# Performance work log

Measured on AMD Instinct MI355X. Metric: run time of the kernel, lower is better.

The kernel has to match this reference:

```python
import jax, jax.numpy as jnp
import numpy as np

B, D, K, A = 32768, 256, 1024, 32
MIN_LOG_STD, MAX_LOG_STD = -20.0, 2.0


def setup_inputs() -> dict:
    key = jax.random.key(0)
    ks = jax.random.split(key, 9)
    return {
        "obs": jax.random.normal(ks[0], (B, D), dtype=jnp.float32),
        "mean_C": jax.random.normal(ks[1], (K, D), dtype=jnp.float32),
        "mean_sigma": jnp.abs(jax.random.normal(ks[2], (K,), dtype=jnp.float32)) + 0.1,
        "mean_w": jax.random.normal(ks[3], (A, K), dtype=jnp.float32),
        "mean_b": jax.random.normal(ks[4], (A,), dtype=jnp.float32),
        "std_C": jax.random.normal(ks[5], (K, D), dtype=jnp.float32),
        "std_sigma": jnp.abs(jax.random.normal(ks[6], (K,), dtype=jnp.float32)) + 0.1,
        "std_w": jax.random.normal(ks[7], (A, K), dtype=jnp.float32),
        "std_b": jax.random.normal(ks[8], (A,), dtype=jnp.float32),
    }


def _rbf(x, C, sigma_sq, w, b):
    # r[b,k] = sum_d (x[b,d] - C[k,d])^2, expanded to avoid a [B,K,D] intermediate
    x2 = jnp.sum(x * x, axis=-1, keepdims=True)           # [B,1]
    c2 = jnp.sum(C * C, axis=-1)[None, :]                  # [1,K]
    r = x2 - 2.0 * (x @ C.T) + c2                          # [B,K]
    phi = jnp.exp(-r / (2.0 * jnp.abs(sigma_sq)[None, :]))  # [B,K]
    return phi @ w.T + b[None, :]                          # [B,A]


def reference(obs, mean_C, mean_sigma, mean_w, mean_b,
              std_C, std_sigma, std_w, std_b):
    action_mean = _rbf(obs, mean_C, mean_sigma, mean_w, mean_b)
    std_raw = _rbf(obs, std_C, std_sigma, std_w, std_b)
    action_std = jnp.exp(jnp.clip(std_raw, MIN_LOG_STD, MAX_LOG_STD))
    return jnp.concatenate((action_mean, action_std), axis=-1)  # [B, 2A]
```

## Files before the change

kernel.cpp:

```cpp
#include <hip/hip_runtime.h>


typedef float floatx4 __attribute__((ext_vector_type(4)));
typedef unsigned int u32;
typedef unsigned char u8;

constexpr float LOG2E = 1.4426950408889634f;

__device__ __forceinline__ u32 pk_fp8(float a, float b, float c, float d) {
  u32 v = __builtin_amdgcn_cvt_pk_fp8_f32(a, b, 0u, 0);
  v = __builtin_amdgcn_cvt_pk_fp8_f32(c, d, v, 1);
  return v;
}
__device__ __forceinline__ long mk64(u32 lo, u32 hi) {
  return (long)lo | ((long)hi << 32);
}

__global__ void prep(const float* __restrict__ mC, const float* __restrict__ mS,
                     const float* __restrict__ sC, const float* __restrict__ sS,
                     const float* __restrict__ mw, const float* __restrict__ sw,
                     u8* __restrict__ Cb, float* __restrict__ a2g,
                     float* __restrict__ g2n, u8* __restrict__ wb)
{
  const int blk = blockIdx.x;
  if (blk < 512) {
    const int wv = threadIdx.x >> 6;
    const int l  = threadIdx.x & 63;
    const int b  = blk * 4 + wv;
    const int half = b >> 10;
    const int k = b & 1023;
    const float* src = (half ? sC : mC) + (size_t)k * 256;
    float4 f = *(const float4*)(src + l * 4);
    float ss = f.x*f.x + f.y*f.y + f.z*f.z + f.w*f.w;
    ((u32*)Cb)[b * 64 + l] = pk_fp8(f.x, f.y, f.z, f.w);
    for (int off = 32; off > 0; off >>= 1) ss += __shfl_down(ss, off, 64);
    if (l == 0) {
      float sig = fabsf((half ? sS : mS)[k]);
      float s2 = LOG2E * 0.5f / sig;
      a2g[b] = 2.f * s2;
      g2n[b] = -s2 * ss;
    }
  } else {
    int i0 = (blk - 512) * 1024 + threadIdx.x * 4;
    int half = i0 >> 15;
    int rem  = i0 & 32767;
    const float* src = half ? sw : mw;
    float4 f = *(const float4*)(src + rem);
    ((u32*)wb)[i0 >> 2] = pk_fp8(f.x, f.y, f.z, f.w);
  }
}

__global__ __launch_bounds__(256, 2)
void policy_main(const float* __restrict__ obs,
                 const u8* __restrict__ Cb,
                 const float* __restrict__ a2g,
                 const float* __restrict__ g2n,
                 const u8* __restrict__ wb,
                 const float* __restrict__ mbias,
                 const float* __restrict__ sbias,
                 float* __restrict__ out)
{
  __shared__ __align__(16) char smem[69888];
  float* x2p = (float*)(smem + 65536);
  float* red = (float*)smem;

  const int tid  = threadIdx.x;
  const int lane = tid & 63;
  const int wv   = tid >> 6;
  const int c    = lane & 15;
  const int q    = lane >> 4;
  const int row0 = blockIdx.x * 64;
  const int crow = 16 * wv + c;
  const int kslc = 16 * wv + 4 * q;
  const int ldl  = tid * 16;

  int goff[4];
  #pragma unroll
  for (int i = 0; i < 4; ++i) {
    int s = i * 256 + tid;
    int row = s >> 4;
    int l16 = (s & 15) ^ (row & 15);
    goff[i] = row * 256 + l16 * 16;
  }

  #pragma unroll
  for (int i = 0; i < 4; ++i) {
    __builtin_amdgcn_global_load_lds(
        (const __attribute__((address_space(1))) u32*)(const void*)(Cb + goff[i]),
        (__attribute__((address_space(3))) u32*)(void*)(smem + i * 4096 + ldl), 16, 0, 0);
    __builtin_amdgcn_global_load_lds(
        (const __attribute__((address_space(1))) u32*)(const void*)(Cb + 16384 + goff[i]),
        (__attribute__((address_space(3))) u32*)(void*)(smem + 16384 + i * 4096 + ldl), 16, 0, 0);
  }

  #pragma unroll
  for (int i = 0; i < 4; ++i) {
    int s = i * 256 + tid;
    int row = s >> 4;
    int s16 = s & 15;
    int l16 = s16 ^ (row & 15);
    const float* src = obs + (size_t)(row0 + row) * 256 + l16 * 16;
    float4 f0 = ((const float4*)src)[0];
    float4 f1 = ((const float4*)src)[1];
    float4 f2 = ((const float4*)src)[2];
    float4 f3 = ((const float4*)src)[3];
    uint4 pk;
    pk.x = pk_fp8(f0.x, f0.y, f0.z, f0.w);
    pk.y = pk_fp8(f1.x, f1.y, f1.z, f1.w);
    pk.z = pk_fp8(f2.x, f2.y, f2.z, f2.w);
    pk.w = pk_fp8(f3.x, f3.y, f3.z, f3.w);
    *(uint4*)(smem + 49152 + s * 16) = pk;
    float p = f0.x*f0.x + f0.y*f0.y + f0.z*f0.z + f0.w*f0.w
            + f1.x*f1.x + f1.y*f1.y + f1.z*f1.z + f1.w*f1.w
            + f2.x*f2.x + f2.y*f2.y + f2.z*f2.z + f2.w*f2.w
            + f3.x*f3.x + f3.y*f3.y + f3.z*f3.z + f3.w*f3.w;
    x2p[row * 16 + s16] = p;
  }
  __syncthreads();

  long ob[4][8];
  #pragma unroll
  for (int nt = 0; nt < 4; ++nt) {
    const int row = nt * 16 + c;
    #pragma unroll
    for (int ks = 0; ks < 8; ++ks) {
      int cc8 = 4 * ks + q;
      int s16 = (cc8 >> 1) ^ (row & 15);
      ob[nt][ks] = *(const long*)(smem + 49152 + row * 256 + s16 * 16 + (q & 1) * 8);
    }
  }
  if (tid < 64) {
    float s = 0.f;
    #pragma unroll
    for (int j = 0; j < 16; j += 4) {
      float4 a = *(const float4*)(x2p + tid * 16 + j);
      s += a.x + a.y + a.z + a.w;
    }
    x2p[1024 + tid] = s;
  }
  __syncthreads();

  float hx2[4];
  #pragma unroll
  for (int nt = 0; nt < 4; ++nt) hx2[nt] = 0.5f * x2p[1024 + nt * 16 + c];

  int voff[8];
  #pragma unroll
  for (int ks = 0; ks < 8; ++ks) {
    int cc8 = 4 * ks + q;
    int s16 = (cc8 >> 1) ^ (crow & 15);
    voff[ks] = crow * 256 + s16 * 16 + (q & 1) * 8;
  }

  const floatx4 Z4 = {0.f, 0.f, 0.f, 0.f};
  floatx4 acc2m[2][4], acc2s[2][4];
  #pragma unroll
  for (int a2i = 0; a2i < 2; ++a2i)
    #pragma unroll
    for (int nt = 0; nt < 4; ++nt) {
      acc2m[a2i][nt] = Z4;
      acc2s[a2i][nt] = Z4;
    }

  int cA = 0, cB = 16384, nA = 32768, nB = 49152;
  u32 pE[4], pc[4];

#define PAIR_BODY(ACC, HB)                                                              \
  {                                                                                     \
    const int cte = 2 * pr;                                                             \
    if (pr < 15) {                                                                      \
      const u8* g0 = Cb + (size_t)(cte + 2) * 16384;                                    \
      _Pragma("unroll")                                                                 \
      for (int i = 0; i < 4; ++i) {                                                     \
        __builtin_amdgcn_global_load_lds(                                               \
            (const __attribute__((address_space(1))) u32*)(const void*)(g0 + goff[i]),  \
            (__attribute__((address_space(3))) u32*)(void*)(smem + nA + i * 4096 + ldl),\
            16, 0, 0);                                                                  \
        __builtin_amdgcn_global_load_lds(                                               \
            (const __attribute__((address_space(1))) u32*)(const void*)(g0 + 16384 + goff[i]), \
            (__attribute__((address_space(3))) u32*)(void*)(smem + nB + i * 4096 + ldl),\
            16, 0, 0);                                                                  \
      }                                                                                 \
    }                                                                                   \
    float4 a2e = *(const float4*)(a2g + cte * 64 + kslc);                               \
    float4 g2e = *(const float4*)(g2n + cte * 64 + kslc);                               \
    float4 a2o = *(const float4*)(a2g + cte * 64 + 64 + kslc);                          \
    float4 g2o = *(const float4*)(g2n + cte * 64 + 64 + kslc);                          \
    const int kbE = (cte & 15) * 64 + kslc;                                             \
    const u8* wr0 = wb + (size_t)(HB + c) * 1024 + kbE;                                 \
    const u8* wr1 = wb + (size_t)(HB + 16 + c) * 1024 + kbE;                            \
    u32 w0lo = *(const u32*)wr0, w0hi = *(const u32*)(wr0 + 64);                        \
    u32 w1lo = *(const u32*)wr1, w1hi = *(const u32*)(wr1 + 64);                        \
    floatx4 a1[4];                                                                      \
    { long cf = *(const long*)(smem + cA + voff[0]);                                    \
      _Pragma("unroll")                                                                 \
      for (int nt = 0; nt < 4; ++nt)                                                    \
        a1[nt] = __builtin_amdgcn_mfma_f32_16x16x32_fp8_fp8(cf, ob[nt][0], Z4, 0, 0, 0); } \
    _Pragma("unroll")                                                                   \
    for (int ks = 1; ks < 8; ++ks) {                                                    \
      long cf = *(const long*)(smem + cA + voff[ks]);                                   \
      _Pragma("unroll")                                                                 \
      for (int nt = 0; nt < 4; ++nt)                                                    \
        a1[nt] = __builtin_amdgcn_mfma_f32_16x16x32_fp8_fp8(cf, ob[nt][ks], a1[nt], 0, 0, 0); \
    }                                                                                   \
    _Pragma("unroll")                                                                   \
    for (int nt = 0; nt < 4; ++nt) {                                                    \
      float t0 = a1[nt][0] - hx2[nt], t1 = a1[nt][1] - hx2[nt];                         \
      float t2 = a1[nt][2] - hx2[nt], t3 = a1[nt][3] - hx2[nt];                         \
      pE[nt] = pk_fp8(__builtin_amdgcn_exp2f(fmaf(a2e.x, t0, g2e.x)),                   \
                      __builtin_amdgcn_exp2f(fmaf(a2e.y, t1, g2e.y)),                   \
                      __builtin_amdgcn_exp2f(fmaf(a2e.z, t2, g2e.z)),                   \
                      __builtin_amdgcn_exp2f(fmaf(a2e.w, t3, g2e.w)));                  \
    }                                                                                   \
    { long cf = *(const long*)(smem + cB + voff[0]);                                    \
      _Pragma("unroll")                                                                 \
      for (int nt = 0; nt < 4; ++nt)                                                    \
        a1[nt] = __builtin_amdgcn_mfma_f32_16x16x32_fp8_fp8(cf, ob[nt][0], Z4, 0, 0, 0); } \
    _Pragma("unroll")                                                                   \
    for (int ks = 1; ks < 8; ++ks) {                                                    \
      long cf = *(const long*)(smem + cB + voff[ks]);                                   \
      _Pragma("unroll")                                                                 \
      for (int nt = 0; nt < 4; ++nt)                                                    \
        a1[nt] = __builtin_amdgcn_mfma_f32_16x16x32_fp8_fp8(cf, ob[nt][ks], a1[nt], 0, 0, 0); \
    }                                                                                   \
    _Pragma("unroll")                                                                   \
    for (int nt = 0; nt < 4; ++nt) {                                                    \
      float t0 = a1[nt][0] - hx2[nt], t1 = a1[nt][1] - hx2[nt];                         \
      float t2 = a1[nt][2] - hx2[nt], t3 = a1[nt][3] - hx2[nt];                         \
      pc[nt] = pk_fp8(__builtin_amdgcn_exp2f(fmaf(a2o.x, t0, g2o.x)),                   \
                      __builtin_amdgcn_exp2f(fmaf(a2o.y, t1, g2o.y)),                   \
                      __builtin_amdgcn_exp2f(fmaf(a2o.z, t2, g2o.z)),                   \
                      __builtin_amdgcn_exp2f(fmaf(a2o.w, t3, g2o.w)));                  \
    }                                                                                   \
    { long wA0 = mk64(w0lo, w0hi), wA1 = mk64(w1lo, w1hi);                              \
      _Pragma("unroll")                                                                 \
      for (int nt = 0; nt < 4; ++nt) {                                                  \
        long pb = mk64(pE[nt], pc[nt]);                                                 \
        ACC[0][nt] = __builtin_amdgcn_mfma_f32_16x16x32_fp8_fp8(wA0, pb, ACC[0][nt], 0, 0, 0); \
        ACC[1][nt] = __builtin_amdgcn_mfma_f32_16x16x32_fp8_fp8(wA1, pb, ACC[1][nt], 0, 0, 0); \
      } }                                                                               \
    __syncthreads();                                                                    \
    { int t_ = cA; cA = nA; nA = t_; t_ = cB; cB = nB; nB = t_; }                       \
  }

  for (int pr = 0; pr < 8; ++pr) PAIR_BODY(acc2m, 0)
  for (int pr = 8; pr < 16; ++pr) PAIR_BODY(acc2s, 32)
#undef PAIR_BODY

  {
    float* myr = red + wv * 4352;
    #pragma unroll
    for (int a2i = 0; a2i < 2; ++a2i)
      #pragma unroll
      for (int nt = 0; nt < 4; ++nt) {
        *(floatx4*)(myr + (nt * 16 + c) * 68 + a2i * 16 + 4 * q)      = acc2m[a2i][nt];
        *(floatx4*)(myr + (nt * 16 + c) * 68 + 32 + a2i * 16 + 4 * q) = acc2s[a2i][nt];
      }
  }
  __syncthreads();

  #pragma unroll
  for (int i = 0; i < 16; ++i) {
    int idx = tid + 256 * i;
    int a = idx & 63;
    int b = idx >> 6;
    float v = red[b * 68 + a] + red[4352 + b * 68 + a] +
              red[8704 + b * 68 + a] + red[13056 + b * 68 + a];
    if (a < 32) {
      v += mbias[a];
    } else {
      v += sbias[a - 32];
      v = fminf(fmaxf(v, -20.f), 2.f);
      v = __builtin_amdgcn_exp2f(v * LOG2E);
    }
    out[(size_t)(row0 + b) * 64 + a] = v;
  }
}

extern "C" void kernel_launch(void* const* d_in, const int* in_sizes, int n_in,
                              void* d_out, int out_size, void* d_ws, size_t ws_size,
                              hipStream_t stream) {
  const float* obs = (const float*)d_in[0];
  const float* mC  = (const float*)d_in[1];
  const float* mS  = (const float*)d_in[2];
  const float* mW  = (const float*)d_in[3];
  const float* mB  = (const float*)d_in[4];
  const float* sC  = (const float*)d_in[5];
  const float* sS  = (const float*)d_in[6];
  const float* sW  = (const float*)d_in[7];
  const float* sB  = (const float*)d_in[8];
  float* out = (float*)d_out;

  u8*    Cb  = (u8*)d_ws;
  float* a2g = (float*)((char*)d_ws + 2048 * 256);
  float* g2n = a2g + 2048;
  u8*    wb  = (u8*)(g2n + 2048);

  prep<<<576, 256, 0, stream>>>(mC, mS, sC, sS, mW, sW, Cb, a2g, g2n, wb);
  policy_main<<<512, 256, 0, stream>>>(obs, Cb, a2g, g2n, wb, mB, sB, out);
}
```

Measured before the change: 133.2 us.

## Split each block's 64 rows across two wave halves using 512 threads

Doubles the block to 8 waves. Each pair of waves shares a 16-wide K slice and each wave handles 32 of the 64 batch rows instead of all 64, so per-wave register state (ob, accumulators) is halved and more waves can hide latency. The LDS prefetch and reduction indexing are reworked for the new wave layout. The cost is that every C fragment is now loaded from LDS by two waves, and there is more synchronisation across a larger block. Occupancy is still capped by LDS at about two blocks per CU, regardless of the launch bound of 4.

```diff
diff --git a/kernel.cpp b/kernel.cpp
--- a/kernel.cpp
+++ b/kernel.cpp
@@ -50,7 +50,7 @@
   }
 }
 
-__global__ __launch_bounds__(256, 2)
+__global__ __launch_bounds__(512, 4)
 void policy_main(const float* __restrict__ obs,
                  const u8* __restrict__ Cb,
                  const float* __restrict__ a2g,
@@ -70,32 +70,34 @@
   const int c    = lane & 15;
   const int q    = lane >> 4;
   const int row0 = blockIdx.x * 64;
-  const int crow = 16 * wv + c;
-  const int kslc = 16 * wv + 4 * q;
+  const int kcs  = 16 * (wv >> 1);
+  const int bh   = 32 * (wv & 1);
+  const int crow = kcs + c;
+  const int kslc = kcs + 4 * q;
   const int ldl  = tid * 16;
 
-  int goff[4];
-  #pragma unroll
-  for (int i = 0; i < 4; ++i) {
-    int s = i * 256 + tid;
+  int goff[2];
+  #pragma unroll
+  for (int i = 0; i < 2; ++i) {
+    int s = i * 512 + tid;
     int row = s >> 4;
     int l16 = (s & 15) ^ (row & 15);
     goff[i] = row * 256 + l16 * 16;
   }
 
   #pragma unroll
-  for (int i = 0; i < 4; ++i) {
+  for (int i = 0; i < 2; ++i) {
     __builtin_amdgcn_global_load_lds(
         (const __attribute__((address_space(1))) u32*)(const void*)(Cb + goff[i]),
-        (__attribute__((address_space(3))) u32*)(void*)(smem + i * 4096 + ldl), 16, 0, 0);
+        (__attribute__((address_space(3))) u32*)(void*)(smem + i * 8192 + ldl), 16, 0, 0);
     __builtin_amdgcn_global_load_lds(
         (const __attribute__((address_space(1))) u32*)(const void*)(Cb + 16384 + goff[i]),
-        (__attribute__((address_space(3))) u32*)(void*)(smem + 16384 + i * 4096 + ldl), 16, 0, 0);
-  }
-
-  #pragma unroll
-  for (int i = 0; i < 4; ++i) {
-    int s = i * 256 + tid;
+        (__attribute__((address_space(3))) u32*)(void*)(smem + 16384 + i * 8192 + ldl), 16, 0, 0);
+  }
+
+  #pragma unroll
+  for (int i = 0; i < 2; ++i) {
+    int s = i * 512 + tid;
     int row = s >> 4;
     int s16 = s & 15;
     int l16 = s16 ^ (row & 15);
@@ -118,10 +120,10 @@
   }
   __syncthreads();
 
-  long ob[4][8];
-  #pragma unroll
-  for (int nt = 0; nt < 4; ++nt) {
-    const int row = nt * 16 + c;
+  long ob[2][8];
+  #pragma unroll
+  for (int nt = 0; nt < 2; ++nt) {
+    const int row = bh + nt * 16 + c;
     #pragma unroll
     for (int ks = 0; ks < 8; ++ks) {
       int cc8 = 4 * ks + q;
@@ -140,9 +142,9 @@
   }
   __syncthreads();
 
-  float hx2[4];
-  #pragma unroll
-  for (int nt = 0; nt < 4; ++nt) hx2[nt] = 0.5f * x2p[1024 + nt * 16 + c];
+  float hx2[2];
+  #pragma unroll
+  for (int nt = 0; nt < 2; ++nt) hx2[nt] = 0.5f * x2p[1024 + bh + nt * 16 + c];
 
   int voff[8];
   #pragma unroll
@@ -153,17 +155,17 @@
   }
 
   const floatx4 Z4 = {0.f, 0.f, 0.f, 0.f};
-  floatx4 acc2m[2][4], acc2s[2][4];
+  floatx4 acc2m[2][2], acc2s[2][2];
   #pragma unroll
   for (int a2i = 0; a2i < 2; ++a2i)
     #pragma unroll
-    for (int nt = 0; nt < 4; ++nt) {
+    for (int nt = 0; nt < 2; ++nt) {
       acc2m[a2i][nt] = Z4;
       acc2s[a2i][nt] = Z4;
     }
 
   int cA = 0, cB = 16384, nA = 32768, nB = 49152;
-  u32 pE[4], pc[4];
+  u32 pE[2], pc[2];
 
 #define PAIR_BODY(ACC, HB)                                                              \
   {                                                                                     \
@@ -171,14 +173,14 @@
     if (pr < 15) {                                                                      \
       const u8* g0 = Cb + (size_t)(cte + 2) * 16384;                                    \
       _Pragma("unroll")                                                                 \
-      for (int i = 0; i < 4; ++i) {                                                     \
+      for (int i = 0; i < 2; ++i) {                                                     \
         __builtin_amdgcn_global_load_lds(                                               \
             (const __attribute__((address_space(1))) u32*)(const void*)(g0 + goff[i]),  \
-            (__attribute__((address_space(3))) u32*)(void*)(smem + nA + i * 4096 + ldl),\
+            (__attribute__((address_space(3))) u32*)(void*)(smem + nA + i * 8192 + ldl),\
             16, 0, 0);                                                                  \
         __builtin_amdgcn_global_load_lds(                                               \
             (const __attribute__((address_space(1))) u32*)(const void*)(g0 + 16384 + goff[i]), \
-            (__attribute__((address_space(3))) u32*)(void*)(smem + nB + i * 4096 + ldl),\
+            (__attribute__((address_space(3))) u32*)(void*)(smem + nB + i * 8192 + ldl),\
             16, 0, 0);                                                                  \
       }                                                                                 \
     }                                                                                   \
@@ -191,20 +193,18 @@
     const u8* wr1 = wb + (size_t)(HB + 16 + c) * 1024 + kbE;                            \
     u32 w0lo = *(const u32*)wr0, w0hi = *(const u32*)(wr0 + 64);                        \
     u32 w1lo = *(const u32*)wr1, w1hi = *(const u32*)(wr1 + 64);                        \
-    floatx4 a1[4];                                                                      \
+    floatx4 a1[2];                                                                      \
     { long cf = *(const long*)(smem + cA + voff[0]);                                    \
-      _Pragma("unroll")                                                                 \
-      for (int nt = 0; nt < 4; ++nt)                                                    \
-        a1[nt] = __builtin_amdgcn_mfma_f32_16x16x32_fp8_fp8(cf, ob[nt][0], Z4, 0, 0, 0); } \
+      a1[0] = __builtin_amdgcn_mfma_f32_16x16x32_fp8_fp8(cf, ob[0][0], Z4, 0, 0, 0);    \
+      a1[1] = __builtin_amdgcn_mfma_f32_16x16x32_fp8_fp8(cf, ob[1][0], Z4, 0, 0, 0); }  \
     _Pragma("unroll")                                                                   \
     for (int ks = 1; ks < 8; ++ks) {                                                    \
       long cf = *(const long*)(smem + cA + voff[ks]);                                   \
-      _Pragma("unroll")                                                                 \
-      for (int nt = 0; nt < 4; ++nt)                                                    \
-        a1[nt] = __builtin_amdgcn_mfma_f32_16x16x32_fp8_fp8(cf, ob[nt][ks], a1[nt], 0, 0, 0); \
+      a1[0] = __builtin_amdgcn_mfma_f32_16x16x32_fp8_fp8(cf, ob[0][ks], a1[0], 0, 0, 0);\
+      a1[1] = __builtin_amdgcn_mfma_f32_16x16x32_fp8_fp8(cf, ob[1][ks], a1[1], 0, 0, 0);\
     }                                                                                   \
     _Pragma("unroll")                                                                   \
-    for (int nt = 0; nt < 4; ++nt) {                                                    \
+    for (int nt = 0; nt < 2; ++nt) {                                                    \
       float t0 = a1[nt][0] - hx2[nt], t1 = a1[nt][1] - hx2[nt];                         \
       float t2 = a1[nt][2] - hx2[nt], t3 = a1[nt][3] - hx2[nt];                         \
       pE[nt] = pk_fp8(__builtin_amdgcn_exp2f(fmaf(a2e.x, t0, g2e.x)),                   \
@@ -213,18 +213,16 @@
                       __builtin_amdgcn_exp2f(fmaf(a2e.w, t3, g2e.w)));                  \
     }                                                                                   \
     { long cf = *(const long*)(smem + cB + voff[0]);                                    \
-      _Pragma("unroll")                                                                 \
-      for (int nt = 0; nt < 4; ++nt)                                                    \
-        a1[nt] = __builtin_amdgcn_mfma_f32_16x16x32_fp8_fp8(cf, ob[nt][0], Z4, 0, 0, 0); } \
+      a1[0] = __builtin_amdgcn_mfma_f32_16x16x32_fp8_fp8(cf, ob[0][0], Z4, 0, 0, 0);    \
+      a1[1] = __builtin_amdgcn_mfma_f32_16x16x32_fp8_fp8(cf, ob[1][0], Z4, 0, 0, 0); }  \
     _Pragma("unroll")                                                                   \
     for (int ks = 1; ks < 8; ++ks) {                                                    \
       long cf = *(const long*)(smem + cB + voff[ks]);                                   \
-      _Pragma("unroll")                                                                 \
-      for (int nt = 0; nt < 4; ++nt)                                                    \
-        a1[nt] = __builtin_amdgcn_mfma_f32_16x16x32_fp8_fp8(cf, ob[nt][ks], a1[nt], 0, 0, 0); \
+      a1[0] = __builtin_amdgcn_mfma_f32_16x16x32_fp8_fp8(cf, ob[0][ks], a1[0], 0, 0, 0);\
+      a1[1] = __builtin_amdgcn_mfma_f32_16x16x32_fp8_fp8(cf, ob[1][ks], a1[1], 0, 0, 0);\
     }                                                                                   \
     _Pragma("unroll")                                                                   \
-    for (int nt = 0; nt < 4; ++nt) {                                                    \
+    for (int nt = 0; nt < 2; ++nt) {                                                    \
       float t0 = a1[nt][0] - hx2[nt], t1 = a1[nt][1] - hx2[nt];                         \
       float t2 = a1[nt][2] - hx2[nt], t3 = a1[nt][3] - hx2[nt];                         \
       pc[nt] = pk_fp8(__builtin_amdgcn_exp2f(fmaf(a2o.x, t0, g2o.x)),                   \
@@ -234,7 +232,7 @@
     }                                                                                   \
     { long wA0 = mk64(w0lo, w0hi), wA1 = mk64(w1lo, w1hi);                              \
       _Pragma("unroll")                                                                 \
-      for (int nt = 0; nt < 4; ++nt) {                                                  \
+      for (int nt = 0; nt < 2; ++nt) {                                                  \
         long pb = mk64(pE[nt], pc[nt]);                                                 \
         ACC[0][nt] = __builtin_amdgcn_mfma_f32_16x16x32_fp8_fp8(wA0, pb, ACC[0][nt], 0, 0, 0); \
         ACC[1][nt] = __builtin_amdgcn_mfma_f32_16x16x32_fp8_fp8(wA1, pb, ACC[1][nt], 0, 0, 0); \
@@ -248,11 +246,11 @@
 #undef PAIR_BODY
 
   {
-    float* myr = red + wv * 4352;
+    float* myr = red + wv * 2176;
     #pragma unroll
     for (int a2i = 0; a2i < 2; ++a2i)
       #pragma unroll
-      for (int nt = 0; nt < 4; ++nt) {
+      for (int nt = 0; nt < 2; ++nt) {
         *(floatx4*)(myr + (nt * 16 + c) * 68 + a2i * 16 + 4 * q)      = acc2m[a2i][nt];
         *(floatx4*)(myr + (nt * 16 + c) * 68 + 32 + a2i * 16 + 4 * q) = acc2s[a2i][nt];
       }
@@ -260,12 +258,14 @@
   __syncthreads();
 
   #pragma unroll
-  for (int i = 0; i < 16; ++i) {
-    int idx = tid + 256 * i;
+  for (int i = 0; i < 8; ++i) {
+    int idx = tid + 512 * i;
     int a = idx & 63;
     int b = idx >> 6;
-    float v = red[b * 68 + a] + red[4352 + b * 68 + a] +
-              red[8704 + b * 68 + a] + red[13056 + b * 68 + a];
+    int bl = b & 31;
+    int w0 = (b >> 5);
+    float v = red[(w0    ) * 2176 + bl * 68 + a] + red[(w0 + 2) * 2176 + bl * 68 + a] +
+              red[(w0 + 4) * 2176 + bl * 68 + a] + red[(w0 + 6) * 2176 + bl * 68 + a];
     if (a < 32) {
       v += mbias[a];
     } else {
@@ -297,5 +297,5 @@
   u8*    wb  = (u8*)(g2n + 2048);
 
   prep<<<576, 256, 0, stream>>>(mC, mS, sC, sS, mW, sW, Cb, a2g, g2n, wb);
-  policy_main<<<512, 256, 0, stream>>>(obs, Cb, a2g, g2n, wb, mB, sB, out);
-}
+  policy_main<<<512, 512, 0, stream>>>(obs, Cb, a2g, g2n, wb, mB, sB, out);
+}
```

Measured after the change: 138.4 us. 3.9% more time.

## Load fp8 centers directly into registers in fragment-order layout, drop LDS staging

Applied to the files above, without the earlier changes.

The prep kernel now writes the fp8 center matrix in a per-thread MFMA fragment order, so each thread can fetch its operand fragments with contiguous 16-byte global loads into registers. The main loop prefetches the next tile pair into a second register set, alternating ping-pong buffers, instead of staging through LDS with global_load_lds. This removes the per-iteration __syncthreads and the LDS reads of centers. In exchange it costs 32 more longs of registers per thread, which may pressure occupancy at launch_bounds(256,2), and global latency is now exposed directly to the waves.

```diff
diff --git a/kernel.cpp b/kernel.cpp
--- a/kernel.cpp
+++ b/kernel.cpp
@@ -2,6 +2,7 @@
 
 
 typedef float floatx4 __attribute__((ext_vector_type(4)));
+typedef long longx2 __attribute__((ext_vector_type(2)));
 typedef unsigned int u32;
 typedef unsigned char u8;
 
@@ -19,22 +20,26 @@
 __global__ void prep(const float* __restrict__ mC, const float* __restrict__ mS,
                      const float* __restrict__ sC, const float* __restrict__ sS,
                      const float* __restrict__ mw, const float* __restrict__ sw,
-                     u8* __restrict__ Cb, float* __restrict__ a2g,
+                     u8* __restrict__ Cb2, float* __restrict__ a2g,
                      float* __restrict__ g2n, u8* __restrict__ wb)
 {
   const int blk = blockIdx.x;
   if (blk < 512) {
-    const int wv = threadIdx.x >> 6;
-    const int l  = threadIdx.x & 63;
-    const int b  = blk * 4 + wv;
+    const int wq = threadIdx.x >> 6;
+    const int t  = threadIdx.x & 63;
+    const int b  = blk * 4 + wq;
     const int half = b >> 10;
     const int k = b & 1023;
     const float* src = (half ? sC : mC) + (size_t)k * 256;
-    float4 f = *(const float4*)(src + l * 4);
+    float4 f = *(const float4*)(src + t * 4);
     float ss = f.x*f.x + f.y*f.y + f.z*f.z + f.w*f.w;
-    ((u32*)Cb)[b * 64 + l] = pk_fp8(f.x, f.y, f.z, f.w);
+    const int ct = b >> 6, row = b & 63;
+    const int wvv = row >> 4, cc = row & 15;
+    const int ks = t >> 3, qq = (t >> 1) & 3, rr = (t & 1) * 4;
+    *(u32*)(Cb2 + (size_t)ct * 16384 + wvv * 4096 + (qq * 16 + cc) * 64 + ks * 8 + rr) =
+        pk_fp8(f.x, f.y, f.z, f.w);
     for (int off = 32; off > 0; off >>= 1) ss += __shfl_down(ss, off, 64);
-    if (l == 0) {
+    if (t == 0) {
       float sig = fabsf((half ? sS : mS)[k]);
       float s2 = LOG2E * 0.5f / sig;
       a2g[b] = 2.f * s2;
@@ -52,7 +57,7 @@
 
 __global__ __launch_bounds__(256, 2)
 void policy_main(const float* __restrict__ obs,
-                 const u8* __restrict__ Cb,
+                 const u8* __restrict__ Cb2,
                  const float* __restrict__ a2g,
                  const float* __restrict__ g2n,
                  const u8* __restrict__ wb,
@@ -61,7 +66,7 @@
                  float* __restrict__ out)
 {
   __shared__ __align__(16) char smem[69888];
-  float* x2p = (float*)(smem + 65536);
+  float* x2p = (float*)(smem + 16384);
   float* red = (float*)smem;
 
   const int tid  = threadIdx.x;
@@ -70,27 +75,16 @@
   const int c    = lane & 15;
   const int q    = lane >> 4;
   const int row0 = blockIdx.x * 64;
-  const int crow = 16 * wv + c;
   const int kslc = 16 * wv + 4 * q;
-  const int ldl  = tid * 16;
-
-  int goff[4];
+  const int cfo  = tid * 64;
+
+  long cfPA[8], cfPB[8], cfQA[8], cfQB[8];
   #pragma unroll
   for (int i = 0; i < 4; ++i) {
-    int s = i * 256 + tid;
-    int row = s >> 4;
-    int l16 = (s & 15) ^ (row & 15);
-    goff[i] = row * 256 + l16 * 16;
-  }
-
-  #pragma unroll
-  for (int i = 0; i < 4; ++i) {
-    __builtin_amdgcn_global_load_lds(
-        (const __attribute__((address_space(1))) u32*)(const void*)(Cb + goff[i]),
-        (__attribute__((address_space(3))) u32*)(void*)(smem + i * 4096 + ldl), 16, 0, 0);
-    __builtin_amdgcn_global_load_lds(
-        (const __attribute__((address_space(1))) u32*)(const void*)(Cb + 16384 + goff[i]),
-        (__attribute__((address_space(3))) u32*)(void*)(smem + 16384 + i * 4096 + ldl), 16, 0, 0);
+    longx2 t0 = *(const longx2*)(Cb2 + cfo + i * 16);
+    cfPA[2 * i] = t0.x; cfPA[2 * i + 1] = t0.y;
+    longx2 t1 = *(const longx2*)(Cb2 + 16384 + cfo + i * 16);
+    cfPB[2 * i] = t1.x; cfPB[2 * i + 1] = t1.y;
   }
 
   #pragma unroll
@@ -109,7 +103,7 @@
     pk.y = pk_fp8(f1.x, f1.y, f1.z, f1.w);
     pk.z = pk_fp8(f2.x, f2.y, f2.z, f2.w);
     pk.w = pk_fp8(f3.x, f3.y, f3.z, f3.w);
-    *(uint4*)(smem + 49152 + s * 16) = pk;
+    *(uint4*)(smem + s * 16) = pk;
     float p = f0.x*f0.x + f0.y*f0.y + f0.z*f0.z + f0.w*f0.w
             + f1.x*f1.x + f1.y*f1.y + f1.z*f1.z + f1.w*f1.w
             + f2.x*f2.x + f2.y*f2.y + f2.z*f2.z + f2.w*f2.w
@@ -126,7 +120,7 @@
     for (int ks = 0; ks < 8; ++ks) {
       int cc8 = 4 * ks + q;
       int s16 = (cc8 >> 1) ^ (row & 15);
-      ob[nt][ks] = *(const long*)(smem + 49152 + row * 256 + s16 * 16 + (q & 1) * 8);
+      ob[nt][ks] = *(const long*)(smem + row * 256 + s16 * 16 + (q & 1) * 8);
     }
   }
   if (tid < 64) {
@@ -144,14 +138,6 @@
   #pragma unroll
   for (int nt = 0; nt < 4; ++nt) hx2[nt] = 0.5f * x2p[1024 + nt * 16 + c];
 
-  int voff[8];
-  #pragma unroll
-  for (int ks = 0; ks < 8; ++ks) {
-    int cc8 = 4 * ks + q;
-    int s16 = (cc8 >> 1) ^ (crow & 15);
-    voff[ks] = crow * 256 + s16 * 16 + (q & 1) * 8;
-  }
-
   const floatx4 Z4 = {0.f, 0.f, 0.f, 0.f};
   floatx4 acc2m[2][4], acc2s[2][4];
   #pragma unroll
@@ -162,24 +148,19 @@
       acc2s[a2i][nt] = Z4;
     }
 
-  int cA = 0, cB = 16384, nA = 32768, nB = 49152;
   u32 pE[4], pc[4];
 
-#define PAIR_BODY(ACC, HB)                                                              \
+#define PAIR_BODY(pr, CA, CB, NA, NB, ACC, HB)                                          \
   {                                                                                     \
-    const int cte = 2 * pr;                                                             \
-    if (pr < 15) {                                                                      \
-      const u8* g0 = Cb + (size_t)(cte + 2) * 16384;                                    \
+    const int cte = 2 * (pr);                                                           \
+    if ((pr) < 15) {                                                                    \
+      const u8* g0 = Cb2 + (size_t)(cte + 2) * 16384 + cfo;                             \
       _Pragma("unroll")                                                                 \
       for (int i = 0; i < 4; ++i) {                                                     \
-        __builtin_amdgcn_global_load_lds(                                               \
-            (const __attribute__((address_space(1))) u32*)(const void*)(g0 + goff[i]),  \
-            (__attribute__((address_space(3))) u32*)(void*)(smem + nA + i * 4096 + ldl),\
-            16, 0, 0);                                                                  \
-        __builtin_amdgcn_global_load_lds(                                               \
-            (const __attribute__((address_space(1))) u32*)(const void*)(g0 + 16384 + goff[i]), \
-            (__attribute__((address_space(3))) u32*)(void*)(smem + nB + i * 4096 + ldl),\
-            16, 0, 0);                                                                  \
+        longx2 t0 = *(const longx2*)(g0 + i * 16);                                      \
+        NA[2 * i] = t0.x; NA[2 * i + 1] = t0.y;                                         \
+        longx2 t1 = *(const longx2*)(g0 + 16384 + i * 16);                              \
+        NB[2 * i] = t1.x; NB[2 * i + 1] = t1.y;                                         \
       }                                                                                 \
     }                                                                                   \
     float4 a2e = *(const float4*)(a2g + cte * 64 + kslc);                               \
@@ -187,21 +168,21 @@
     float4 a2o = *(const float4*)(a2g + cte * 64 + 64 + kslc);                          \
     float4 g2o = *(const float4*)(g2n + cte * 64 + 64 + kslc);                          \
     const int kbE = (cte & 15) * 64 + kslc;                                             \
-    const u8* wr0 = wb + (size_t)(HB + c) * 1024 + kbE;                                 \
-    const u8* wr1 = wb + (size_t)(HB + 16 + c) * 1024 + kbE;                            \
+    const u8* wr0 = wb + (size_t)((HB) + c) * 1024 + kbE;                               \
+    const u8* wr1 = wb + (size_t)((HB) + 16 + c) * 1024 + kbE;                          \
     u32 w0lo = *(const u32*)wr0, w0hi = *(const u32*)(wr0 + 64);                        \
     u32 w1lo = *(const u32*)wr1, w1hi = *(const u32*)(wr1 + 64);                        \
     floatx4 a1[4];                                                                      \
-    { long cf = *(const long*)(smem + cA + voff[0]);                                    \
-      _Pragma("unroll")                                                                 \
-      for (int nt = 0; nt < 4; ++nt)                                                    \
-        a1[nt] = __builtin_amdgcn_mfma_f32_16x16x32_fp8_fp8(cf, ob[nt][0], Z4, 0, 0, 0); } \
+    a1[0] = __builtin_amdgcn_mfma_f32_16x16x32_fp8_fp8(CA[0], ob[0][0], Z4, 0, 0, 0);   \
+    a1[1] = __builtin_amdgcn_mfma_f32_16x16x32_fp8_fp8(CA[0], ob[1][0], Z4, 0, 0, 0);   \
+    a1[2] = __builtin_amdgcn_mfma_f32_16x16x32_fp8_fp8(CA[0], ob[2][0], Z4, 0, 0, 0);   \
+    a1[3] = __builtin_amdgcn_mfma_f32_16x16x32_fp8_fp8(CA[0], ob[3][0], Z4, 0, 0, 0);   \
     _Pragma("unroll")                                                                   \
     for (int ks = 1; ks < 8; ++ks) {                                                    \
-      long cf = *(const long*)(smem + cA + voff[ks]);                                   \
-      _Pragma("unroll")                                                                 \
-      for (int nt = 0; nt < 4; ++nt)                                                    \
-        a1[nt] = __builtin_amdgcn_mfma_f32_16x16x32_fp8_fp8(cf, ob[nt][ks], a1[nt], 0, 0, 0); \
+      a1[0] = __builtin_amdgcn_mfma_f32_16x16x32_fp8_fp8(CA[ks], ob[0][ks], a1[0], 0, 0, 0); \
+      a1[1] = __builtin_amdgcn_mfma_f32_16x16x32_fp8_fp8(CA[ks], ob[1][ks], a1[1], 0, 0, 0); \
+      a1[2] = __builtin_amdgcn_mfma_f32_16x16x32_fp8_fp8(CA[ks], ob[2][ks], a1[2], 0, 0, 0); \
+      a1[3] = __builtin_amdgcn_mfma_f32_16x16x32_fp8_fp8(CA[ks], ob[3][ks], a1[3], 0, 0, 0); \
     }                                                                                   \
     _Pragma("unroll")                                                                   \
     for (int nt = 0; nt < 4; ++nt) {                                                    \
@@ -212,16 +193,16 @@
                       __builtin_amdgcn_exp2f(fmaf(a2e.z, t2, g2e.z)),                   \
                       __builtin_amdgcn_exp2f(fmaf(a2e.w, t3, g2e.w)));                  \
     }                                                                                   \
-    { long cf = *(const long*)(smem + cB + voff[0]);                                    \
-      _Pragma("unroll")                                                                 \
-      for (int nt = 0; nt < 4; ++nt)                                                    \
-        a1[nt] = __builtin_amdgcn_mfma_f32_16x16x32_fp8_fp8(cf, ob[nt][0], Z4, 0, 0, 0); } \
+    a1[0] = __builtin_amdgcn_mfma_f32_16x16x32_fp8_fp8(CB[0], ob[0][0], Z4, 0, 0, 0);   \
+    a1[1] = __builtin_amdgcn_mfma_f32_16x16x32_fp8_fp8(CB[0], ob[1][0], Z4, 0, 0, 0);   \
+    a1[2] = __builtin_amdgcn_mfma_f32_16x16x32_fp8_fp8(CB[0], ob[2][0], Z4, 0, 0, 0);   \
+    a1[3] = __builtin_amdgcn_mfma_f32_16x16x32_fp8_fp8(CB[0], ob[3][0], Z4, 0, 0, 0);   \
     _Pragma("unroll")                                                                   \
     for (int ks = 1; ks < 8; ++ks) {                                                    \
-      long cf = *(const long*)(smem + cB + voff[ks]);                                   \
-      _Pragma("unroll")                                                                 \
-      for (int nt = 0; nt < 4; ++nt)                                                    \
-        a1[nt] = __builtin_amdgcn_mfma_f32_16x16x32_fp8_fp8(cf, ob[nt][ks], a1[nt], 0, 0, 0); \
+      a1[0] = __builtin_amdgcn_mfma_f32_16x16x32_fp8_fp8(CB[ks], ob[0][ks], a1[0], 0, 0, 0); \
+      a1[1] = __builtin_amdgcn_mfma_f32_16x16x32_fp8_fp8(CB[ks], ob[1][ks], a1[1], 0, 0, 0); \
+      a1[2] = __builtin_amdgcn_mfma_f32_16x16x32_fp8_fp8(CB[ks], ob[2][ks], a1[2], 0, 0, 0); \
+      a1[3] = __builtin_amdgcn_mfma_f32_16x16x32_fp8_fp8(CB[ks], ob[3][ks], a1[3], 0, 0, 0); \
     }                                                                                   \
     _Pragma("unroll")                                                                   \
     for (int nt = 0; nt < 4; ++nt) {                                                    \
@@ -239,12 +220,16 @@
         ACC[0][nt] = __builtin_amdgcn_mfma_f32_16x16x32_fp8_fp8(wA0, pb, ACC[0][nt], 0, 0, 0); \
         ACC[1][nt] = __builtin_amdgcn_mfma_f32_16x16x32_fp8_fp8(wA1, pb, ACC[1][nt], 0, 0, 0); \
       } }                                                                               \
-    __syncthreads();                                                                    \
-    { int t_ = cA; cA = nA; nA = t_; t_ = cB; cB = nB; nB = t_; }                       \
-  }
-
-  for (int pr = 0; pr < 8; ++pr) PAIR_BODY(acc2m, 0)
-  for (int pr = 8; pr < 16; ++pr) PAIR_BODY(acc2s, 32)
+  }
+
+  for (int pr = 0; pr < 8; pr += 2) {
+    PAIR_BODY(pr,     cfPA, cfPB, cfQA, cfQB, acc2m, 0)
+    PAIR_BODY(pr + 1, cfQA, cfQB, cfPA, cfPB, acc2m, 0)
+  }
+  for (int pr = 8; pr < 16; pr += 2) {
+    PAIR_BODY(pr,     cfPA, cfPB, cfQA, cfQB, acc2s, 32)
+    PAIR_BODY(pr + 1, cfQA, cfQB, cfPA, cfPB, acc2s, 32)
+  }
 #undef PAIR_BODY
 
   {
@@ -291,11 +276,11 @@
   const float* sB  = (const float*)d_in[8];
   float* out = (float*)d_out;
 
-  u8*    Cb  = (u8*)d_ws;
+  u8*    Cb2 = (u8*)d_ws;
   float* a2g = (float*)((char*)d_ws + 2048 * 256);
   float* g2n = a2g + 2048;
   u8*    wb  = (u8*)(g2n + 2048);
 
-  prep<<<576, 256, 0, stream>>>(mC, mS, sC, sS, mW, sW, Cb, a2g, g2n, wb);
-  policy_main<<<512, 256, 0, stream>>>(obs, Cb, a2g, g2n, wb, mB, sB, out);
-}
+  prep<<<576, 256, 0, stream>>>(mC, mS, sC, sS, mW, sW, Cb2, a2g, g2n, wb);
+  policy_main<<<512, 256, 0, stream>>>(obs, Cb2, a2g, g2n, wb, mB, sB, out);
+}
```

After: 130.1 us. 2.3% less time.
